# Kernel optimization log

Measured on AMD Instinct MI355X. Metric: run time of the kernel, lower is better.

Reference implementation:

```python
import jax, jax.numpy as jnp
import numpy as np

N_SRC = 50000   # source nodes in the block
N_DST = 50000   # destination nodes
E = 800000      # edges (avg in-degree 16, every dst has >=1 edge)
D = 256         # hidden_dim
V = 50000       # vocab_size
C = 104         # n_classes (POJ-104)


def setup_inputs() -> dict:
    key = jax.random.key(0)
    k1, k2, k3, k4, k5, k6 = jax.random.split(key, 6)
    token_id = jax.random.randint(k1, (N_SRC,), 0, V, dtype=jnp.int32)
    src_idx = jax.random.randint(k2, (E,), 0, N_SRC, dtype=jnp.int32)
    # every dst node gets at least one in-edge (DGL raises on 0-in-degree),
    # remaining edges land on random dst nodes; sorted so edges are grouped by dst
    extra = jax.random.randint(k3, (E - N_DST,), 0, N_DST, dtype=jnp.int32)
    dst_idx = jnp.sort(jnp.concatenate([jnp.arange(N_DST, dtype=jnp.int32), extra]))
    emb = jax.random.normal(k4, (V, D), dtype=jnp.float32)  # nn.Embedding default N(0,1)
    W = jax.random.normal(k5, (D, D), dtype=jnp.float32) / jnp.sqrt(D)
    b = jnp.zeros((D,), dtype=jnp.float32)
    Wc = jax.random.normal(k6, (C, D), dtype=jnp.float32) / jnp.sqrt(D)
    bc = jnp.zeros((C,), dtype=jnp.float32)
    return {"emb": emb, "W": W, "b": b, "Wc": Wc, "bc": bc,
            "token_id": token_id, "src_idx": src_idx, "dst_idx": dst_idx}


def reference(emb, W, b, Wc, bc, token_id, src_idx, dst_idx):
    # embedding gather for source nodes (first_layer branch)
    feat_src = emb[token_id]                  # [N_SRC, D]
    # message: copy_u -> mailbox messages per edge
    msgs = feat_src[src_idx]                  # [E, D]
    # per-dst segment stats (dst_idx is sorted / grouped by dst)
    deg = jax.ops.segment_sum(jnp.ones((E,), dtype=jnp.int32), dst_idx,
                              num_segments=N_DST)            # [N_DST]
    sum_all = jax.ops.segment_sum(msgs, dst_idx, num_segments=N_DST)  # [N_DST, D]
    # DGL mailbox reducer: last message in the segment is the 'current input',
    # the rest are children summed through CodeRNNCell: x = cur + relu(W @ sum_children + b)
    last_idx = jnp.cumsum(deg) - 1            # index of last edge per dst segment
    last_msg = msgs[last_idx]                 # [N_DST, D]
    child_sum = sum_all - last_msg            # sum of msgs excluding the last one
    rnn_out = last_msg + jax.nn.relu(child_sum @ W.T + b)
    # length == 1 segments bypass the RNN cell entirely: ft = the single message
    ft = jnp.where((deg == 1)[:, None], last_msg, rnn_out)   # [N_DST, D]
    # final classifier
    return ft @ Wc.T + bc                     # [N_DST, C]
```

## Files before the change

kernel.cpp:

```cpp
#include <hip/hip_runtime.h>
#include <hip/hip_bf16.h>

#define DD 256
#define CC 104
#define NSL 8

typedef __bf16 bf16x8 __attribute__((ext_vector_type(8)));
typedef float  f32x4  __attribute__((ext_vector_type(4)));
typedef unsigned u32x2 __attribute__((ext_vector_type(2)));

__device__ inline float bu2f(unsigned short u) {
    return __uint_as_float(((unsigned)u) << 16);
}
__device__ inline unsigned short f2bu(float f) {
    __hip_bfloat16 h = __float2bfloat16(f);
    return *reinterpret_cast<unsigned short*>(&h);
}

__global__ void prep_all(
    const int* __restrict__ token_id,
    const int* __restrict__ src_idx,
    const int* __restrict__ dst_idx,
    int* __restrict__ seg_start,
    int* __restrict__ seg_end,
    int* __restrict__ etp,
    int* __restrict__ last_tok,
    int E, int PB,
    const float* __restrict__ W,
    const float* __restrict__ Wc,
    __hip_bfloat16* __restrict__ Wfrag,
    __hip_bfloat16* __restrict__ Wcfrag)
{
    const int b = blockIdx.x;
    const int t = threadIdx.x;
    if (b < PB) {
        int e = b * 256 + t;
        if (e >= E) return;
        int d = dst_idx[e];
        int tok = token_id[src_idx[e]];
        int lastf = (e == E - 1 || dst_idx[e + 1] != d) ? 1 : 0;
        etp[e] = tok | ((d & 15) << 16) | (lastf << 20);
        if (e == 0 || dst_idx[e - 1] != d) seg_start[d] = e;
        if (lastf) { seg_end[d] = e + 1; last_tok[d] = tok; }
        return;
    }
    if (b < PB + 32) {
        int idx  = (b - PB) * 256 + t;
        int lane = idx & 63, g = idx >> 6;
        int nt = g & 15, k0 = g >> 4;
        int r = nt * 16 + (lane & 15);
        int c = k0 * 32 + (lane >> 4) * 8;
        const float* src = W + (size_t)r * DD + c;
        float4 v0 = *(const float4*)(src);
        float4 v1 = *(const float4*)(src + 4);
        uint4 pk;
        pk.x = (unsigned)f2bu(v0.x) | ((unsigned)f2bu(v0.y) << 16);
        pk.y = (unsigned)f2bu(v0.z) | ((unsigned)f2bu(v0.w) << 16);
        pk.z = (unsigned)f2bu(v1.x) | ((unsigned)f2bu(v1.y) << 16);
        pk.w = (unsigned)f2bu(v1.z) | ((unsigned)f2bu(v1.w) << 16);
        *(uint4*)(Wfrag + (size_t)idx * 8) = pk;
        return;
    }
    {
        int idx  = (b - PB - 32) * 256 + t;
        int lane = idx & 63, g = idx >> 6;
        int nt = g & 7, k0 = g >> 3;
        int r = nt * 16 + (lane & 15);
        int c = k0 * 32 + (lane >> 4) * 8;
        float4 v0 = make_float4(0.f,0.f,0.f,0.f);
        float4 v1 = make_float4(0.f,0.f,0.f,0.f);
        if (r < CC) {
            const float* src = Wc + (size_t)r * DD + c;
            v0 = *(const float4*)(src);
            v1 = *(const float4*)(src + 4);
        }
        uint4 pk;
        pk.x = (unsigned)f2bu(v0.x) | ((unsigned)f2bu(v0.y) << 16);
        pk.y = (unsigned)f2bu(v0.z) | ((unsigned)f2bu(v0.w) << 16);
        pk.z = (unsigned)f2bu(v1.x) | ((unsigned)f2bu(v1.y) << 16);
        pk.w = (unsigned)f2bu(v1.z) | ((unsigned)f2bu(v1.w) << 16);
        *(uint4*)(Wcfrag + (size_t)idx * 8) = pk;
    }
}

__global__ __launch_bounds__(256, 3) void we_gemm(
    const float* __restrict__ emb,
    const __hip_bfloat16* __restrict__ Wfrag,
    __hip_bfloat16* __restrict__ Webuf,
    __hip_bfloat16* __restrict__ embb,
    int V)
{
    __shared__ __hip_bfloat16 lds[32 * 512];
    const int t    = threadIdx.x;
    const int lane = t & 63;
    const int w    = t >> 6;
    const int quad = lane >> 4;
    const int l16  = lane & 15;
    const int mrow = blockIdx.x * 64 + w * 16 + l16;
    const int row  = min(mrow, V - 1);

    bf16x8 bfrag[8];
#pragma unroll
    for (int k0 = 0; k0 < 8; ++k0) {
        const float* src = emb + (size_t)row * DD + k0 * 32 + quad * 8;
        float4 v0 = *(const float4*)(src);
        float4 v1 = *(const float4*)(src + 4);
        uint4 pk;
        pk.x = (unsigned)f2bu(v0.x) | ((unsigned)f2bu(v0.y) << 16);
        pk.y = (unsigned)f2bu(v0.z) | ((unsigned)f2bu(v0.w) << 16);
        pk.z = (unsigned)f2bu(v1.x) | ((unsigned)f2bu(v1.y) << 16);
        pk.w = (unsigned)f2bu(v1.z) | ((unsigned)f2bu(v1.w) << 16);
        bfrag[k0] = *(bf16x8*)&pk;
        if (mrow < V)
            *(uint4*)(embb + (size_t)k0 * V * 32 + (size_t)row * 32 + quad * 8) = pk;
    }

    f32x4 acc[16];
#pragma unroll
    for (int nt = 0; nt < 16; ++nt) acc[nt] = (f32x4){0.f,0.f,0.f,0.f};

    for (int p = 0; p < 4; ++p) {
        if (p) __syncthreads();
#pragma unroll
        for (int it = 0; it < 8; ++it) {
            int idx = it * 256 + t;
            *(uint4*)(lds + (size_t)idx * 8) =
                *(const uint4*)(Wfrag + (size_t)p * 16384 + (size_t)idx * 8);
        }
        __syncthreads();
#pragma unroll
        for (int kl = 0; kl < 2; ++kl) {
            int k0 = p * 2 + kl;
#pragma unroll
            for (int nt = 0; nt < 16; ++nt) {
                bf16x8 wf = *(const bf16x8*)(lds + (kl * 16 + nt) * 512 + lane * 8);
                acc[nt] = __builtin_amdgcn_mfma_f32_16x16x32_bf16(wf, bfrag[k0], acc[nt], 0, 0, 0);
            }
        }
    }

    if (mrow < V) {
#pragma unroll
        for (int nt = 0; nt < 16; ++nt) {
            int c0 = nt * 16 + quad * 4;
            ushort4 o;
            o.x = f2bu(acc[nt][0]);
            o.y = f2bu(acc[nt][1]);
            o.z = f2bu(acc[nt][2]);
            o.w = f2bu(acc[nt][3]);
            *(ushort4*)(Webuf + (size_t)(c0 >> 5) * V * 32 +
                        (size_t)mrow * 32 + (c0 & 31)) = o;
        }
    }
}

__global__ __launch_bounds__(256, 4) void seg_mfma(
    const __hip_bfloat16* __restrict__ Webuf,
    const __hip_bfloat16* __restrict__ embb,
    const int* __restrict__ etp,
    const int* __restrict__ seg_start,
    const int* __restrict__ seg_end,
    const int* __restrict__ last_tok,
    const float* __restrict__ bvec,
    __hip_bfloat16* __restrict__ ftb,
    int n_dst, int V, int E)
{
    __shared__ unsigned char      ldsT[4][2][2048];
    __shared__ unsigned long long ldsC[4][2][4];
    const int t   = threadIdx.x;
    const int wv  = t >> 6;
    const int l   = t & 63;
    const int sl  = blockIdx.x & 7;
    const int g   = (blockIdx.x >> 3) * 4 + wv;
    const int d0  = g * 16;
    if (d0 >= n_dst) return;
    const int d1  = min(d0 + 16, n_dst);
    const int S   = seg_start[d0];
    const int End = seg_end[d1 - 1];
    const int l15 = l & 15;
    const int k   = l >> 1;
    const int half= l & 1;
    const int sp   = (k >> 2) & 1;
    const int srho = ((k >> 3) << 2) | (k & 3);
    const unsigned woff  = (unsigned)(half * 1024 + sp * 512 + srho * 32);
    const unsigned troff = (unsigned)(((l >> 4) << 7) + (l15 << 3));
    const __hip_bfloat16* wsl = Webuf + (size_t)sl * V * 32;
    const __hip_bfloat16* esl = embb  + (size_t)sl * V * 32;

    f32x4 acc0 = {0.f,0.f,0.f,0.f};
    f32x4 acc1 = {0.f,0.f,0.f,0.f};
    const int R = (End - S + 31) >> 5;
    const int rmax = R - 1;

    uint4 Q0, Q1; int code;
    auto GATHER = [&](int r, uint4& A0, uint4& A1, int& cd) {
        int e  = S + 32 * r + k;
        int ec = min(e, End - 1);
        int m  = etp[ec];
        int tok = m & 0xFFFF;
        const __hip_bfloat16* src = wsl + (size_t)tok * 32 + half * 16;
        A0 = *(const uint4*)(src);
        A1 = *(const uint4*)(src + 8);
        cd = (e < End && !((m >> 20) & 1)) ? ((m >> 16) & 15) : 255;
    };
    auto WRITE = [&](int buf, const uint4& A0, const uint4& A1, int cd) {
        unsigned char* mb = &ldsT[wv][buf][0];
        *(uint4*)(mb + woff)      = A0;
        *(uint4*)(mb + woff + 16) = A1;
        if (half == 0)
            ((unsigned char*)&ldsC[wv][buf][0])[k] = (unsigned char)cd;
    };

    GATHER(0, Q0, Q1, code);
    WRITE(0, Q0, Q1, code);

    for (int r = 0; r < R; ++r) {
        int rn = min(r + 1, rmax);
        GATHER(rn, Q0, Q1, code);
        __builtin_amdgcn_sched_barrier(0);

        const int buf = r & 1;
        unsigned long long c8 = ldsC[wv][buf][l >> 4];
        unsigned mw0, mw1, mw2, mw3;
        {
            unsigned ul15 = (unsigned)l15;
            mw0 = (((unsigned)(c8 >>  0) & 0xFFu) == ul15 ? 0x3F80u : 0u)
                | (((unsigned)(c8 >>  8) & 0xFFu) == ul15 ? 0x3F800000u : 0u);
            mw1 = (((unsigned)(c8 >> 16) & 0xFFu) == ul15 ? 0x3F80u : 0u)
                | (((unsigned)(c8 >> 24) & 0xFFu) == ul15 ? 0x3F800000u : 0u);
            mw2 = (((unsigned)(c8 >> 32) & 0xFFu) == ul15 ? 0x3F80u : 0u)
                | (((unsigned)(c8 >> 40) & 0xFFu) == ul15 ? 0x3F800000u : 0u);
            mw3 = (((unsigned)(c8 >> 48) & 0xFFu) == ul15 ? 0x3F80u : 0u)
                | (((unsigned)(c8 >> 56) & 0xFFu) == ul15 ? 0x3F800000u : 0u);
        }
        uint4 mq = make_uint4(mw0, mw1, mw2, mw3);
        bf16x8 bm = *(bf16x8*)&mq;

        unsigned base = (unsigned)(uintptr_t)&ldsT[wv][buf][0] + troff;
        u32x2 r00, r01, r10, r11;
        asm volatile(
            "ds_read_b64_tr_b16 %0, %4\n\t"
            "ds_read_b64_tr_b16 %1, %4 offset:512\n\t"
            "ds_read_b64_tr_b16 %2, %4 offset:1024\n\t"
            "ds_read_b64_tr_b16 %3, %4 offset:1536\n\t"
            "s_waitcnt lgkmcnt(0)"
            : "=&v"(r00), "=&v"(r01), "=&v"(r10), "=&v"(r11)
            : "v"(base)
            : "memory");
        __builtin_amdgcn_sched_barrier(0);

        uint4 a0q = make_uint4(r00[0], r00[1], r01[0], r01[1]);
        uint4 a1q = make_uint4(r10[0], r10[1], r11[0], r11[1]);
        bf16x8 am0 = *(bf16x8*)&a0q;
        bf16x8 am1 = *(bf16x8*)&a1q;
        acc0 = __builtin_amdgcn_mfma_f32_16x16x32_bf16(am0, bm, acc0, 0, 0, 0);
        acc1 = __builtin_amdgcn_mfma_f32_16x16x32_bf16(am1, bm, acc1, 0, 0, 0);

        WRITE((r + 1) & 1, Q0, Q1, code);
    }

    int dst = d0 + l15;
    bool dok = dst < n_dst;
    int dc = min(dst, n_dst - 1);
    int lt  = last_tok[dc];
    int nch = seg_end[dc] - seg_start[dc] - 1;
    bool gate = nch > 0;
    int q = (l >> 4) * 4;
    ushort4 lm0 = *(const ushort4*)(esl + (size_t)lt * 32 + q);
    ushort4 lm1 = *(const ushort4*)(esl + (size_t)lt * 32 + 16 + q);
    float4 b0 = *(const float4*)(bvec + sl * 32 + q);
    float4 b1 = *(const float4*)(bvec + sl * 32 + 16 + q);
    ushort4 o0, o1;
    o0.x = f2bu(bu2f(lm0.x) + (gate ? fmaxf(acc0[0] + b0.x, 0.f) : 0.f));
    o0.y = f2bu(bu2f(lm0.y) + (gate ? fmaxf(acc0[1] + b0.y, 0.f) : 0.f));
    o0.z = f2bu(bu2f(lm0.z) + (gate ? fmaxf(acc0[2] + b0.z, 0.f) : 0.f));
    o0.w = f2bu(bu2f(lm0.w) + (gate ? fmaxf(acc0[3] + b0.w, 0.f) : 0.f));
    o1.x = f2bu(bu2f(lm1.x) + (gate ? fmaxf(acc1[0] + b1.x, 0.f) : 0.f));
    o1.y = f2bu(bu2f(lm1.y) + (gate ? fmaxf(acc1[1] + b1.y, 0.f) : 0.f));
    o1.z = f2bu(bu2f(lm1.z) + (gate ? fmaxf(acc1[2] + b1.z, 0.f) : 0.f));
    o1.w = f2bu(bu2f(lm1.w) + (gate ? fmaxf(acc1[3] + b1.w, 0.f) : 0.f));
    if (dok) {
        __hip_bfloat16* fb = ftb + (size_t)sl * n_dst * 32 + (size_t)dst * 32;
        *(ushort4*)(fb + q)      = o0;
        *(ushort4*)(fb + 16 + q) = o1;
    }
}

__global__ __launch_bounds__(256, 4) void cls_mfma(
    const __hip_bfloat16* __restrict__ ftb,
    const __hip_bfloat16* __restrict__ Wcfrag,
    const float* __restrict__ bc,
    float* __restrict__ out,
    int M)
{
    __shared__ __hip_bfloat16 lds[32 * 512];
    const int t    = threadIdx.x;
    const int lane = t & 63;
    const int w    = t >> 6;
    const int quad = lane >> 4;
    const int l16  = lane & 15;
    const int mw   = blockIdx.x * 64 + w * 16;

    int mrow = min(mw + l16, M - 1);
    bf16x8 ffrag[8];
#pragma unroll
    for (int k0 = 0; k0 < 8; ++k0)
        ffrag[k0] = *(const bf16x8*)(ftb + (size_t)k0 * M * 32 +
                                     (size_t)mrow * 32 + quad * 8);

    f32x4 acc[8];
#pragma unroll
    for (int nt = 0; nt < 8; ++nt) acc[nt] = (f32x4){0.f,0.f,0.f,0.f};

    for (int p = 0; p < 2; ++p) {
        if (p) __syncthreads();
#pragma unroll
        for (int it = 0; it < 8; ++it) {
            int idx = it * 256 + t;
            *(uint4*)(lds + (size_t)idx * 8) =
                *(const uint4*)(Wcfrag + (size_t)p * 16384 + (size_t)idx * 8);
        }
        __syncthreads();
#pragma unroll
        for (int kl = 0; kl < 4; ++kl) {
            int k0 = p * 4 + kl;
#pragma unroll
            for (int nt = 0; nt < 8; ++nt) {
                bf16x8 wf = *(const bf16x8*)(lds + (kl * 8 + nt) * 512 + lane * 8);
                acc[nt] = __builtin_amdgcn_mfma_f32_16x16x32_bf16(wf, ffrag[k0], acc[nt], 0, 0, 0);
            }
        }
    }

    int m = mw + l16;
    if (m < M) {
#pragma unroll
        for (int nt = 0; nt < 8; ++nt) {
            int c0 = nt * 16 + quad * 4;
            if (c0 <= 100) {
                float4 bia = *(const float4*)(bc + c0);
                float4 o;
                o.x = acc[nt][0] + bia.x;
                o.y = acc[nt][1] + bia.y;
                o.z = acc[nt][2] + bia.z;
                o.w = acc[nt][3] + bia.w;
                *(float4*)(out + (size_t)m * CC + c0) = o;
            }
        }
    }
}

extern "C" void kernel_launch(void* const* d_in, const int* in_sizes, int n_in,
                              void* d_out, int out_size, void* d_ws, size_t ws_size,
                              hipStream_t stream)
{
    const float* emb      = (const float*)d_in[0];
    const float* W        = (const float*)d_in[1];
    const float* bvec     = (const float*)d_in[2];
    const float* Wc       = (const float*)d_in[3];
    const float* bc       = (const float*)d_in[4];
    const int*   token_id = (const int*)d_in[5];
    const int*   src_idx  = (const int*)d_in[6];
    const int*   dst_idx  = (const int*)d_in[7];
    float*       out      = (float*)d_out;

    const int E     = in_sizes[6];
    const int Vemb  = in_sizes[0] / DD;
    const int n_dst = out_size / CC;
    (void)n_in; (void)ws_size;

    char* ws = (char*)d_ws;
    size_t off = 0;
    auto alloc = [&](size_t bytes) {
        void* p = ws + off;
        off = (off + bytes + 255) & ~(size_t)255;
        return p;
    };
    int* seg_start = (int*)alloc((size_t)n_dst * sizeof(int));
    int* seg_end   = (int*)alloc((size_t)n_dst * sizeof(int));
    int* last_tok  = (int*)alloc((size_t)n_dst * sizeof(int));
    int* etp       = (int*)alloc((size_t)E * sizeof(int));
    __hip_bfloat16* embb   = (__hip_bfloat16*)alloc((size_t)Vemb * DD * 2);
    __hip_bfloat16* Webuf  = (__hip_bfloat16*)alloc((size_t)Vemb * DD * 2);
    __hip_bfloat16* ftb    = (__hip_bfloat16*)alloc((size_t)n_dst * DD * 2);
    __hip_bfloat16* Wfrag  = (__hip_bfloat16*)alloc((size_t)128 * 512 * 2);
    __hip_bfloat16* Wcfrag = (__hip_bfloat16*)alloc((size_t)64 * 512 * 2);

    const int PB = (E + 255) / 256;
    const int we_blocks  = (Vemb + 63) / 64;
    const int ngroups    = (n_dst + 15) / 16;
    const int seg_blocks = NSL * ((ngroups + 3) / 4);
    const int cls_blocks = (n_dst + 63) / 64;

    prep_all<<<PB + 48, 256, 0, stream>>>(
        token_id, src_idx, dst_idx, seg_start, seg_end, etp, last_tok, E, PB,
        W, Wc, Wfrag, Wcfrag);
    we_gemm<<<we_blocks, 256, 0, stream>>>(
        emb, Wfrag, Webuf, embb, Vemb);
    seg_mfma<<<seg_blocks, 256, 0, stream>>>(
        Webuf, embb, etp, seg_start, seg_end, last_tok, bvec, ftb,
        n_dst, Vemb, E);
    cls_mfma<<<cls_blocks, 256, 0, stream>>>(
        ftb, Wcfrag, bc, out, n_dst);
}
```

Baseline: 187.8 us.

## Precompute segment one-hot mask fragments in a separate kernel for seg_mfma

Adds a mask_build kernel that writes, for every 32-edge round of each 16-destination group, the bf16 one-hot B fragment each lane needs. seg_mfma then streams these fragments from global memory with nontemporal loads instead of staging per-edge codes in LDS and building the mask with compares. This takes LDS writes and ALU work off the inner loop. In exchange it adds a kernel launch and about 1 KB of mask traffic per round, roughly 25 MB written and read back, eight times over since all eight slices reload the same masks.

```diff
diff --git a/kernel.cpp b/kernel.cpp
--- a/kernel.cpp
+++ b/kernel.cpp
@@ -83,6 +83,41 @@
     }
 }
 
+__global__ __launch_bounds__(256, 8) void mask_build(
+    const int* __restrict__ etp,
+    const int* __restrict__ seg_start,
+    const int* __restrict__ seg_end,
+    uint4* __restrict__ maskbuf,
+    int n_dst)
+{
+    const int g  = blockIdx.x;
+    const int wv = threadIdx.x >> 6;
+    const int l  = threadIdx.x & 63;
+    const int l15 = l & 15;
+    const int kb  = (l >> 4) * 8;
+    const int d0 = g * 16;
+    if (d0 >= n_dst) return;
+    const int d1  = min(d0 + 16, n_dst);
+    const int S   = seg_start[d0];
+    const int End = seg_end[d1 - 1];
+    const int R   = (End - S + 31) >> 5;
+    const int rb  = (S >> 5) + g;
+    for (int r = wv; r < R; r += 4) {
+        int ebase = S + 32 * r + kb;
+        unsigned mw[4] = {0u, 0u, 0u, 0u};
+#pragma unroll
+        for (int j = 0; j < 8; ++j) {
+            int e  = ebase + j;
+            int ec = min(e, End - 1);
+            int m  = etp[ec];
+            bool match = (e < End) && !((m >> 20) & 1)
+                       && (((m >> 16) & 15) == l15);
+            if (match) mw[j >> 1] |= (j & 1) ? 0x3F800000u : 0x3F80u;
+        }
+        maskbuf[(size_t)(rb + r) * 64 + l] = make_uint4(mw[0], mw[1], mw[2], mw[3]);
+    }
+}
+
 __global__ __launch_bounds__(256, 3) void we_gemm(
     const float* __restrict__ emb,
     const __hip_bfloat16* __restrict__ Wfrag,
@@ -161,12 +196,12 @@
     const int* __restrict__ seg_start,
     const int* __restrict__ seg_end,
     const int* __restrict__ last_tok,
+    const uint4* __restrict__ maskbuf,
     const float* __restrict__ bvec,
     __hip_bfloat16* __restrict__ ftb,
-    int n_dst, int V, int E)
-{
-    __shared__ unsigned char      ldsT[4][2][2048];
-    __shared__ unsigned long long ldsC[4][2][4];
+    int n_dst, int V)
+{
+    __shared__ unsigned char ldsT[4][2][2048];
     const int t   = threadIdx.x;
     const int wv  = t >> 6;
     const int l   = t & 63;
@@ -177,6 +212,7 @@
     const int d1  = min(d0 + 16, n_dst);
     const int S   = seg_start[d0];
     const int End = seg_end[d1 - 1];
+    const int rb  = (S >> 5) + g;
     const int l15 = l & 15;
     const int k   = l >> 1;
     const int half= l & 1;
@@ -192,8 +228,8 @@
     const int R = (End - S + 31) >> 5;
     const int rmax = R - 1;
 
-    uint4 Q0, Q1; int code;
-    auto GATHER = [&](int r, uint4& A0, uint4& A1, int& cd) {
+    uint4 Q0, Q1;
+    auto GATHER = [&](int r, uint4& A0, uint4& A1) {
         int e  = S + 32 * r + k;
         int ec = min(e, End - 1);
         int m  = etp[ec];
@@ -201,41 +237,35 @@
         const __hip_bfloat16* src = wsl + (size_t)tok * 32 + half * 16;
         A0 = *(const uint4*)(src);
         A1 = *(const uint4*)(src + 8);
-        cd = (e < End && !((m >> 20) & 1)) ? ((m >> 16) & 15) : 255;
     };
-    auto WRITE = [&](int buf, const uint4& A0, const uint4& A1, int cd) {
+    auto WRITE = [&](int buf, const uint4& A0, const uint4& A1) {
         unsigned char* mb = &ldsT[wv][buf][0];
         *(uint4*)(mb + woff)      = A0;
         *(uint4*)(mb + woff + 16) = A1;
-        if (half == 0)
-            ((unsigned char*)&ldsC[wv][buf][0])[k] = (unsigned char)cd;
     };
-
-    GATHER(0, Q0, Q1, code);
-    WRITE(0, Q0, Q1, code);
+    auto MLOAD = [&](int r) -> uint4 {
+        const unsigned long long* mp =
+            (const unsigned long long*)(maskbuf + ((size_t)(rb + r) << 6) + l);
+        unsigned long long m0 = __builtin_nontemporal_load(mp);
+        unsigned long long m1 = __builtin_nontemporal_load(mp + 1);
+        uint4 q;
+        ((unsigned long long*)&q)[0] = m0;
+        ((unsigned long long*)&q)[1] = m1;
+        return q;
+    };
+
+    GATHER(0, Q0, Q1);
+    WRITE(0, Q0, Q1);
+    uint4 mq = MLOAD(0);
 
     for (int r = 0; r < R; ++r) {
         int rn = min(r + 1, rmax);
-        GATHER(rn, Q0, Q1, code);
+        GATHER(rn, Q0, Q1);
+        uint4 mqn = MLOAD(rn);
         __builtin_amdgcn_sched_barrier(0);
 
         const int buf = r & 1;
-        unsigned long long c8 = ldsC[wv][buf][l >> 4];
-        unsigned mw0, mw1, mw2, mw3;
-        {
-            unsigned ul15 = (unsigned)l15;
-            mw0 = (((unsigned)(c8 >>  0) & 0xFFu) == ul15 ? 0x3F80u : 0u)
-                | (((unsigned)(c8 >>  8) & 0xFFu) == ul15 ? 0x3F800000u : 0u);
-            mw1 = (((unsigned)(c8 >> 16) & 0xFFu) == ul15 ? 0x3F80u : 0u)
-                | (((unsigned)(c8 >> 24) & 0xFFu) == ul15 ? 0x3F800000u : 0u);
-            mw2 = (((unsigned)(c8 >> 32) & 0xFFu) == ul15 ? 0x3F80u : 0u)
-                | (((unsigned)(c8 >> 40) & 0xFFu) == ul15 ? 0x3F800000u : 0u);
-            mw3 = (((unsigned)(c8 >> 48) & 0xFFu) == ul15 ? 0x3F80u : 0u)
-                | (((unsigned)(c8 >> 56) & 0xFFu) == ul15 ? 0x3F800000u : 0u);
-        }
-        uint4 mq = make_uint4(mw0, mw1, mw2, mw3);
         bf16x8 bm = *(bf16x8*)&mq;
-
         unsigned base = (unsigned)(uintptr_t)&ldsT[wv][buf][0] + troff;
         u32x2 r00, r01, r10, r11;
         asm volatile(
@@ -256,7 +286,8 @@
         acc0 = __builtin_amdgcn_mfma_f32_16x16x32_bf16(am0, bm, acc0, 0, 0, 0);
         acc1 = __builtin_amdgcn_mfma_f32_16x16x32_bf16(am1, bm, acc1, 0, 0, 0);
 
-        WRITE((r + 1) & 1, Q0, Q1, code);
+        WRITE((r + 1) & 1, Q0, Q1);
+        mq = mqn;
     }
 
     int dst = d0 + l15;
@@ -376,6 +407,8 @@
         off = (off + bytes + 255) & ~(size_t)255;
         return p;
     };
+    const int ngroups = (n_dst + 15) / 16;
+    const size_t mask_slots = (size_t)(E >> 5) + ngroups + 2;
     int* seg_start = (int*)alloc((size_t)n_dst * sizeof(int));
     int* seg_end   = (int*)alloc((size_t)n_dst * sizeof(int));
     int* last_tok  = (int*)alloc((size_t)n_dst * sizeof(int));
@@ -385,21 +418,23 @@
     __hip_bfloat16* ftb    = (__hip_bfloat16*)alloc((size_t)n_dst * DD * 2);
     __hip_bfloat16* Wfrag  = (__hip_bfloat16*)alloc((size_t)128 * 512 * 2);
     __hip_bfloat16* Wcfrag = (__hip_bfloat16*)alloc((size_t)64 * 512 * 2);
+    uint4* maskbuf = (uint4*)alloc(mask_slots * 1024);
 
     const int PB = (E + 255) / 256;
     const int we_blocks  = (Vemb + 63) / 64;
-    const int ngroups    = (n_dst + 15) / 16;
     const int seg_blocks = NSL * ((ngroups + 3) / 4);
     const int cls_blocks = (n_dst + 63) / 64;
 
     prep_all<<<PB + 48, 256, 0, stream>>>(
         token_id, src_idx, dst_idx, seg_start, seg_end, etp, last_tok, E, PB,
         W, Wc, Wfrag, Wcfrag);
+    mask_build<<<ngroups, 256, 0, stream>>>(
+        etp, seg_start, seg_end, maskbuf, n_dst);
     we_gemm<<<we_blocks, 256, 0, stream>>>(
         emb, Wfrag, Webuf, embb, Vemb);
     seg_mfma<<<seg_blocks, 256, 0, stream>>>(
-        Webuf, embb, etp, seg_start, seg_end, last_tok, bvec, ftb,
-        n_dst, Vemb, E);
+        Webuf, embb, etp, seg_start, seg_end, last_tok, maskbuf, bvec, ftb,
+        n_dst, Vemb);
     cls_mfma<<<cls_blocks, 256, 0, stream>>>(
         ftb, Wcfrag, bc, out, n_dst);
 }
```

After: 257.4 us. 1.37x slower.
